# Performance work log

Hardware: AMD Instinct MI355X
Metric: run time of the kernel (lower is better)

The kernel has to match this reference:

```python
import jax, jax.numpy as jnp
import numpy as np

MAX_EDGE_LENGTH = 100.0  # filtration cap from cfg['self_supervised']['max_edge_length']


def pairwise_dist(x):
    # Euclidean pairwise distances, [N, N]
    sq = jnp.sum(x * x, axis=-1)
    d2 = sq[:, None] + sq[None, :] - 2.0 * (x @ x.T)
    return jnp.sqrt(jnp.maximum(d2, 0.0) + 1e-12)


def mst_edge_weights(D):
    """Prim's MST over dense distance matrix D [N,N]. Returns N-1 edge weights.
    These weights are exactly the H0 death times of the Vietoris-Rips filtration
    (all H0 features are born at 0)."""
    N = D.shape[0]
    dist0 = D[0]                                   # min distance from tree to each node
    in_tree0 = jnp.zeros((N,), bool).at[0].set(True)

    def step(carry, _):
        dist, in_tree = carry
        masked = jnp.where(in_tree, jnp.inf, dist)
        j = jnp.argmin(masked)
        w = masked[j]                              # weight of edge added to MST
        in_tree = in_tree.at[j].set(True)
        dist = jnp.minimum(dist, D[j])
        return (dist, in_tree), w

    _, weights = jax.lax.scan(step, (dist0, in_tree0), None, length=N - 1)
    return weights


def h0_deaths(x):
    # H0 persistence diagram deaths (births are all 0), capped at max_edge_length
    return jnp.minimum(mst_edge_weights(pairwise_dist(x)), MAX_EDGE_LENGTH)


def setup_inputs() -> dict:
    key = jax.random.key(0)
    k1, k2 = jax.random.split(key)
    N, Dm = 4096, 128
    x_1 = jax.random.normal(k1, (N, Dm), dtype=jnp.float32)
    # correlated second view, as in a siamese/self-supervised setting
    x_2 = x_1 + 0.1 * jax.random.normal(k2, (N, Dm), dtype=jnp.float32)
    return {"x_1": x_1, "x_2": x_2, "plot": 0}


def reference(x_1, x_2, plot):
    # MSE representation loss
    representation_loss = jnp.mean((x_1 - x_2) ** 2)
    # H0 persistence diagrams via Vietoris-Rips (MST formulation)
    d1 = jnp.sort(h0_deaths(x_1))
    d2 = jnp.sort(h0_deaths(x_2))
    # Wasserstein-1 distance between the two H0 diagrams (births all 0,
    # equal cardinality => optimal matching is the sorted matching of deaths)
    topological_loss = jnp.sum(jnp.abs(d1 - d2))
    return representation_loss + topological_loss
```

## Files before the change

kernel.cpp:

```cpp
#include <hip/hip_runtime.h>
#include <hip/hip_fp16.h>

#define NPT 4096
#define DM 128
#define ROUNDS 12
#define INF64 0xFFFFFFFFFFFFFFFFull
#define INF32 0xFFFFFFFFu

typedef _Float16 f16x8 __attribute__((ext_vector_type(8)));
typedef _Float16 f16x2 __attribute__((ext_vector_type(2)));
typedef float f32x4 __attribute__((ext_vector_type(4)));

static __device__ __forceinline__ unsigned long long make_key64(unsigned key, unsigned node) {
    unsigned h = key >> 16, j = key & 0xFFFFu;
    unsigned mn = node < j ? node : j;
    unsigned mx = node < j ? j : node;
    return ((unsigned long long)h << 48) | ((unsigned long long)mn << 32) |
           ((unsigned long long)mx << 16) | (unsigned long long)j;
}

__global__ __launch_bounds__(256) void init_kernel(unsigned* __restrict__ comp,
                                                   unsigned long long* __restrict__ compbest,
                                                   float* __restrict__ w,
                                                   unsigned* __restrict__ cnt,
                                                   float* __restrict__ rep) {
    int i = blockIdx.x * blockDim.x + threadIdx.x;
    comp[i] = (unsigned)(i & (NPT - 1));
    compbest[i] = INF64;
    w[i] = 0.0f;
    if (i < 2) cnt[i] = 0u;
    if (i == 0) rep[0] = 0.0f;
}

__global__ __launch_bounds__(256) void prep_kernel(const float* __restrict__ x1,
                                                   const float* __restrict__ x2,
                                                   _Float16* __restrict__ Xh,
                                                   float* __restrict__ norms,
                                                   float* __restrict__ rep) {
    const int wv = threadIdx.x >> 6, ln = threadIdx.x & 63;
    const int row = blockIdx.x * 4 + wv;
    float2 v1 = *(const float2*)(x1 + (size_t)row * DM + ln * 2);
    float2 v2 = *(const float2*)(x2 + (size_t)row * DM + ln * 2);
    _Float16 a0 = (_Float16)v1.x, a1 = (_Float16)v1.y;
    _Float16 b0 = (_Float16)v2.x, b1 = (_Float16)v2.y;
    f16x2 pa; pa[0] = a0; pa[1] = a1;
    f16x2 pb; pb[0] = b0; pb[1] = b1;
    *(f16x2*)(Xh + (size_t)row * DM + ln * 2) = pa;
    *(f16x2*)(Xh + (size_t)(NPT + row) * DM + ln * 2) = pb;

    float s1 = (float)a0 * (float)a0 + (float)a1 * (float)a1;
    float s2 = (float)b0 * (float)b0 + (float)b1 * (float)b1;
    float dx = v1.x - v2.x, dy = v1.y - v2.y;
    float rs = dx * dx + dy * dy;
    #pragma unroll
    for (int off = 32; off > 0; off >>= 1) {
        s1 += __shfl_down(s1, off);
        s2 += __shfl_down(s2, off);
        rs += __shfl_down(rs, off);
    }
    __shared__ float partial[4];
    if (ln == 0) {
        norms[row] = s1;
        norms[NPT + row] = s2;
        partial[wv] = rs;
    }
    __syncthreads();
    if (threadIdx.x == 0)
        atomicAdd(rep, partial[0] + partial[1] + partial[2] + partial[3]);
}

__global__ __launch_bounds__(256) void gram_kernel(const _Float16* __restrict__ Xh,
                                                   const float* __restrict__ norms,
                                                   __half* __restrict__ Dall,
                                                   unsigned long long* __restrict__ compbestAll) {
    const int mat = blockIdx.y;
    const _Float16* __restrict__ X = Xh + (size_t)mat * NPT * DM;
    const float* __restrict__ nrm = norms + mat * NPT;
    __half* __restrict__ D = Dall + (size_t)mat * NPT * NPT;
    unsigned long long* __restrict__ compbest = compbestAll + mat * NPT;

    const int I = blockIdx.x >> 5;
    const int J = blockIdx.x & 31;

    __shared__ __half tile[128 * 136];
    __shared__ unsigned keybuf[128 * 33];

    const int t = threadIdx.x;
    const int wv = t >> 6, ln = t & 63;
    const int rloc = (wv >> 1) * 64;
    const int cloc = (wv & 1) * 64;
    const int rowBase = I * 128 + rloc;
    const int colBase = J * 128 + cloc;
    const int lr = ln & 15;
    const int kg = ln >> 4;

    f32x4 acc[4][4];
    #pragma unroll
    for (int m = 0; m < 4; ++m)
        #pragma unroll
        for (int n = 0; n < 4; ++n)
            acc[m][n] = (f32x4){0.f, 0.f, 0.f, 0.f};

    #pragma unroll
    for (int ks = 0; ks < 4; ++ks) {
        const int k0 = ks * 32 + kg * 8;
        f16x8 a[4], b[4];
        #pragma unroll
        for (int m = 0; m < 4; ++m)
            a[m] = *(const f16x8*)(X + (size_t)(rowBase + m * 16 + lr) * DM + k0);
        #pragma unroll
        for (int n = 0; n < 4; ++n)
            b[n] = *(const f16x8*)(X + (size_t)(colBase + n * 16 + lr) * DM + k0);
        #pragma unroll
        for (int m = 0; m < 4; ++m)
            #pragma unroll
            for (int n = 0; n < 4; ++n)
                acc[m][n] = __builtin_amdgcn_mfma_f32_16x16x32_f16(a[m], b[n], acc[m][n], 0, 0, 0);
    }

    float nr[16], nc[4];
    #pragma unroll
    for (int m = 0; m < 4; ++m)
        #pragma unroll
        for (int q = 0; q < 4; ++q)
            nr[m * 4 + q] = nrm[rowBase + m * 16 + kg * 4 + q];
    #pragma unroll
    for (int n = 0; n < 4; ++n) nc[n] = nrm[colBase + n * 16 + lr];

    #pragma unroll
    for (int m = 0; m < 4; ++m) {
        #pragma unroll
        for (int q = 0; q < 4; ++q) {
            const int rl = rloc + m * 16 + kg * 4 + q;
            const int rglob = I * 128 + rl;
            unsigned best = INF32;
            #pragma unroll
            for (int n = 0; n < 4; ++n) {
                const int cl = cloc + n * 16 + lr;
                const int cglob = J * 128 + cl;
                float d2 = nr[m * 4 + q] + nc[n] - 2.0f * acc[m][n][q];
                float d = sqrtf(fmaxf(d2, 0.0f) + 1e-12f);
                __half hd = __float2half(d);
                tile[rl * 136 + cl] = hd;
                unsigned key = ((unsigned)__half_as_ushort(hd) << 16) | (unsigned)cglob;
                if (cglob == rglob) key = INF32;
                best = best < key ? best : key;
            }
            keybuf[rl * 33 + (wv & 1) * 16 + lr] = best;
        }
    }
    __syncthreads();

    {
        const int r = t >> 1, h = t & 1;
        unsigned best = INF32;
        #pragma unroll
        for (int i = 0; i < 16; ++i) {
            unsigned k = keybuf[r * 33 + h * 16 + i];
            best = best < k ? best : k;
        }
        unsigned o = __shfl_xor(best, 1);
        best = best < o ? best : o;
        if (h == 0 && best != INF32)
            atomicMin(&compbest[I * 128 + r], make_key64(best, (unsigned)(I * 128 + r)));
    }

    const int tileRow0 = I * 128;
    #pragma unroll
    for (int it = 0; it < 8; ++it) {
        int idx = it * 256 + t;
        int row = idx >> 4;
        int ch = idx & 15;
        *(uint4*)(&D[(size_t)(tileRow0 + row) * NPT + J * 128 + ch * 8]) =
            *(const uint4*)(&tile[row * 136 + ch * 8]);
    }
}

__global__ __launch_bounds__(1024) void boruvka_a2(const __half* __restrict__ Dall,
                                                   const unsigned* __restrict__ compAll,
                                                   unsigned long long* __restrict__ compbestAll,
                                                   const unsigned* __restrict__ cnt) {
    const int mat = blockIdx.y;
    if (cnt[mat] >= NPT - 1u) return;
    const __half* __restrict__ D = Dall + (size_t)mat * NPT * NPT;
    const unsigned* __restrict__ comp = compAll + mat * NPT;
    unsigned long long* __restrict__ compbest = compbestAll + mat * NPT;

    __shared__ unsigned short lcomp[NPT];
    const int t = threadIdx.x;
    for (int i = t; i < NPT; i += 1024) lcomp[i] = (unsigned short)comp[i];
    __syncthreads();

    const int wv = t >> 6, ln = t & 63;
    const int node0 = blockIdx.x * 32 + wv * 2;
    const int node1 = node0 + 1;
    const unsigned ci0 = lcomp[node0];
    const unsigned ci1 = lcomp[node1];
    const uint4* __restrict__ row0 = (const uint4*)(D + (size_t)node0 * NPT);
    const uint4* __restrict__ row1 = (const uint4*)(D + (size_t)node1 * NPT);

    uint4 d0[8], d1[8];
    #pragma unroll
    for (int k = 0; k < 8; ++k) d0[k] = row0[k * 64 + ln];
    #pragma unroll
    for (int k = 0; k < 8; ++k) d1[k] = row1[k * 64 + ln];

    unsigned best0 = INF32, best1 = INF32;
    #pragma unroll
    for (int k = 0; k < 8; ++k) {
        const int jb = (k * 64 + ln) * 8;
        uint4 cv = *(const uint4*)&lcomp[jb];
        const unsigned dp0[4] = {d0[k].x, d0[k].y, d0[k].z, d0[k].w};
        const unsigned dp1[4] = {d1[k].x, d1[k].y, d1[k].z, d1[k].w};
        const unsigned cp[4]  = {cv.x, cv.y, cv.z, cv.w};
        #pragma unroll
        for (int q = 0; q < 4; ++q) {
            int j0 = jb + q * 2;
            unsigned clo = cp[q] & 0xFFFFu, chi = cp[q] >> 16;
            unsigned k00 = (dp0[q] << 16) | (unsigned)j0;
            unsigned k01 = (dp0[q] & 0xFFFF0000u) | (unsigned)(j0 + 1);
            if (clo == ci0) k00 = INF32;
            if (chi == ci0) k01 = INF32;
            unsigned m0 = k00 < k01 ? k00 : k01;
            best0 = best0 < m0 ? best0 : m0;
            unsigned k10 = (dp1[q] << 16) | (unsigned)j0;
            unsigned k11 = (dp1[q] & 0xFFFF0000u) | (unsigned)(j0 + 1);
            if (clo == ci1) k10 = INF32;
            if (chi == ci1) k11 = INF32;
            unsigned m1 = k10 < k11 ? k10 : k11;
            best1 = best1 < m1 ? best1 : m1;
        }
    }
    #pragma unroll
    for (int off = 32; off > 0; off >>= 1) {
        unsigned o0 = __shfl_down(best0, off);
        best0 = best0 < o0 ? best0 : o0;
        unsigned o1 = __shfl_down(best1, off);
        best1 = best1 < o1 ? best1 : o1;
    }
    if (ln == 0) {
        if (best0 != INF32) atomicMin(&compbest[ci0], make_key64(best0, (unsigned)node0));
        if (best1 != INF32) atomicMin(&compbest[ci1], make_key64(best1, (unsigned)node1));
    }
}

__global__ __launch_bounds__(1024) void boruvka_cd(unsigned* __restrict__ compAll,
                                                   unsigned long long* __restrict__ compbestAll,
                                                   float* __restrict__ wAll,
                                                   unsigned* __restrict__ cntAll) {
    const int mat = blockIdx.x;
    if (cntAll[mat] >= NPT - 1u) return;
    unsigned* __restrict__ comp = compAll + mat * NPT;
    unsigned long long* __restrict__ compbest = compbestAll + mat * NPT;
    float* __restrict__ w = wAll + mat * NPT;
    unsigned* __restrict__ cnt = cntAll + mat;

    __shared__ unsigned short par[NPT];
    const int t = threadIdx.x;

    for (int c = t; c < NPT; c += 1024) {
        unsigned p = (unsigned)c;
        unsigned long long key = compbest[c];
        if (comp[c] == (unsigned)c && key != INF64) {
            unsigned jout = (unsigned)(key & 0xFFFFull);
            unsigned c2 = comp[jout];
            unsigned long long k2 = compbest[c2];
            bool mutual = (k2 >> 16) == (key >> 16);
            if (!mutual || (unsigned)c < c2) {
                unsigned short hb = (unsigned short)(key >> 48);
                float wv = fminf(__half2float(__ushort_as_half(hb)), 100.0f);
                unsigned slot = atomicAdd(cnt, 1u);
                w[slot] = wv;
            }
            p = (mutual && (unsigned)c < c2) ? (unsigned)c : c2;
        }
        par[c] = (unsigned short)p;
    }
    __syncthreads();

    for (int it = 0; it < 12; ++it) {
        unsigned short np[4];
        #pragma unroll
        for (int q = 0; q < 4; ++q) np[q] = par[par[t + q * 1024]];
        __syncthreads();
        #pragma unroll
        for (int q = 0; q < 4; ++q) par[t + q * 1024] = np[q];
        __syncthreads();
    }

    for (int c = t; c < NPT; c += 1024) {
        comp[c] = par[comp[c]];
        compbest[c] = INF64;
    }
}

__global__ __launch_bounds__(1024) void sort_kernel(float* __restrict__ wAll) {
    float* __restrict__ w = wAll + blockIdx.x * NPT;
    __shared__ float s[NPT];
    const int t = threadIdx.x;
    for (int i = t; i < NPT; i += 1024) s[i] = w[i];
    __syncthreads();

    for (int k = 2; k <= NPT; k <<= 1) {
        for (int j = k >> 1; j > 0; j >>= 1) {
            for (int i = t; i < NPT; i += 1024) {
                int ixj = i ^ j;
                if (ixj > i) {
                    bool up = (i & k) == 0;
                    float a = s[i], b = s[ixj];
                    if ((a > b) == up) { s[i] = b; s[ixj] = a; }
                }
            }
            __syncthreads();
        }
    }
    for (int i = t; i < NPT; i += 1024) w[i] = s[i];
}

__global__ __launch_bounds__(1024) void final2_kernel(const float* __restrict__ w,
                                                      const float* __restrict__ rep,
                                                      float* __restrict__ out) {
    const int t = threadIdx.x;
    float loc = 0.f;
    for (int i = t; i < NPT; i += 1024) loc += fabsf(w[i] - w[NPT + i]);
    #pragma unroll
    for (int off = 32; off > 0; off >>= 1) loc += __shfl_down(loc, off);
    __shared__ float reds[16];
    int wv = t >> 6, ln = t & 63;
    if (ln == 0) reds[wv] = loc;
    __syncthreads();
    if (t == 0) {
        float tot = 0.f;
        #pragma unroll
        for (int i = 0; i < 16; ++i) tot += reds[i];
        out[0] = tot + rep[0] * (1.0f / (NPT * DM));
    }
}

extern "C" void kernel_launch(void* const* d_in, const int* in_sizes, int n_in,
                              void* d_out, int out_size, void* d_ws, size_t ws_size,
                              hipStream_t stream) {
    const float* x1 = (const float*)d_in[0];
    const float* x2 = (const float*)d_in[1];
    float* out = (float*)d_out;

    char* ws = (char*)d_ws;
    __half* D = (__half*)ws;
    size_t off = (size_t)2 * NPT * NPT * sizeof(__half);
    _Float16* Xh = (_Float16*)(ws + off);
    off += (size_t)2 * NPT * DM * sizeof(_Float16);
    float* norms = (float*)(ws + off);
    off += (size_t)2 * NPT * sizeof(float);
    unsigned long long* compbest = (unsigned long long*)(ws + off);
    off += (size_t)2 * NPT * sizeof(unsigned long long);
    float* w = (float*)(ws + off);
    off += (size_t)2 * NPT * sizeof(float);
    unsigned* comp = (unsigned*)(ws + off);
    off += (size_t)2 * NPT * sizeof(unsigned);
    unsigned* cnt = (unsigned*)(ws + off);
    off += 2 * sizeof(unsigned);
    float* rep = (float*)(ws + off);

    init_kernel<<<2 * NPT / 256, 256, 0, stream>>>(comp, compbest, w, cnt, rep);

    prep_kernel<<<NPT / 4, 256, 0, stream>>>(x1, x2, Xh, norms, rep);

    gram_kernel<<<dim3(1024, 2), 256, 0, stream>>>(Xh, norms, D, compbest);

    boruvka_cd<<<2, 1024, 0, stream>>>(comp, compbest, w, cnt);

    for (int r = 1; r < ROUNDS; ++r) {
        boruvka_a2<<<dim3(NPT / 32, 2), 1024, 0, stream>>>(D, comp, compbest, cnt);
        boruvka_cd<<<2, 1024, 0, stream>>>(comp, compbest, w, cnt);
    }

    sort_kernel<<<2, 1024, 0, stream>>>(w);

    final2_kernel<<<1, 1024, 0, stream>>>(w, rep, out);
}
```

Before: 347.8 us.

## Track per-node second-best neighbor to skip full Boruvka row scans on alternate rounds

The gram kernel now records, for each row, the two smallest distance keys per column tile. A new reduction kernel turns these into best and second-best candidates per node. Boruvka rounds then alternate between a full row scan that keeps the top two keys in distinct components and a cheap pairA pass. That pass reuses the stored candidates and only rescans the row when both fall inside the node's own component. The aim is to cut the number of full passes over the 2x32MB fp16 distance matrix. In exchange the full scans carry extra per-lane state and shuffle work, and more kernels are launched.

```diff
diff --git a/kernel.cpp b/kernel.cpp
--- a/kernel.cpp
+++ b/kernel.cpp
@@ -3,7 +3,6 @@
 
 #define NPT 4096
 #define DM 128
-#define ROUNDS 12
 #define INF64 0xFFFFFFFFFFFFFFFFull
 #define INF32 0xFFFFFFFFu
 
@@ -18,6 +17,15 @@
     return ((unsigned long long)h << 48) | ((unsigned long long)mn << 32) |
            ((unsigned long long)mx << 16) | (unsigned long long)j;
 }
+
+#define UPD(K1, C1, K2, C2, kk, cc)                                   \
+    do {                                                              \
+        unsigned _k = (kk), _c = (cc);                                \
+        if (_k < K1) {                                                \
+            if (_c != C1) { K2 = K1; C2 = C1; }                       \
+            K1 = _k; C1 = _c;                                         \
+        } else if (_k < K2 && _c != C1) { K2 = _k; C2 = _c; }         \
+    } while (0)
 
 __global__ __launch_bounds__(256) void init_kernel(unsigned* __restrict__ comp,
                                                    unsigned long long* __restrict__ compbest,
@@ -72,18 +80,18 @@
 __global__ __launch_bounds__(256) void gram_kernel(const _Float16* __restrict__ Xh,
                                                    const float* __restrict__ norms,
                                                    __half* __restrict__ Dall,
-                                                   unsigned long long* __restrict__ compbestAll) {
+                                                   unsigned* __restrict__ Gall) {
     const int mat = blockIdx.y;
     const _Float16* __restrict__ X = Xh + (size_t)mat * NPT * DM;
     const float* __restrict__ nrm = norms + mat * NPT;
     __half* __restrict__ D = Dall + (size_t)mat * NPT * NPT;
-    unsigned long long* __restrict__ compbest = compbestAll + mat * NPT;
+    unsigned* __restrict__ G = Gall + (size_t)mat * NPT * 64;
 
     const int I = blockIdx.x >> 5;
     const int J = blockIdx.x & 31;
 
     __shared__ __half tile[128 * 136];
-    __shared__ unsigned keybuf[128 * 33];
+    __shared__ unsigned keybuf[128 * 66];
 
     const int t = threadIdx.x;
     const int wv = t >> 6, ln = t & 63;
@@ -133,7 +141,7 @@
         for (int q = 0; q < 4; ++q) {
             const int rl = rloc + m * 16 + kg * 4 + q;
             const int rglob = I * 128 + rl;
-            unsigned best = INF32;
+            unsigned b = INF32, s = INF32;
             #pragma unroll
             for (int n = 0; n < 4; ++n) {
                 const int cl = cloc + n * 16 + lr;
@@ -144,26 +152,38 @@
                 tile[rl * 136 + cl] = hd;
                 unsigned key = ((unsigned)__half_as_ushort(hd) << 16) | (unsigned)cglob;
                 if (cglob == rglob) key = INF32;
-                best = best < key ? best : key;
+                if (key < b) { s = b; b = key; } else if (key < s) s = key;
             }
-            keybuf[rl * 33 + (wv & 1) * 16 + lr] = best;
+            keybuf[rl * 66 + (wv & 1) * 16 + lr] = b;
+            keybuf[rl * 66 + 33 + (wv & 1) * 16 + lr] = s;
         }
     }
     __syncthreads();
 
     {
         const int r = t >> 1, h = t & 1;
-        unsigned best = INF32;
+        unsigned B = INF32, S = INF32;
         #pragma unroll
         for (int i = 0; i < 16; ++i) {
-            unsigned k = keybuf[r * 33 + h * 16 + i];
-            best = best < k ? best : k;
-        }
-        unsigned o = __shfl_xor(best, 1);
-        best = best < o ? best : o;
-        if (h == 0 && best != INF32)
-            atomicMin(&compbest[I * 128 + r], make_key64(best, (unsigned)(I * 128 + r)));
-    }
+            unsigned k = keybuf[r * 66 + h * 16 + i];
+            if (k < B) { S = B; B = k; } else if (k < S) S = k;
+        }
+        #pragma unroll
+        for (int i = 0; i < 16; ++i) {
+            unsigned k = keybuf[r * 66 + 33 + h * 16 + i];
+            if (k < B) { S = B; B = k; } else if (k < S) S = k;
+        }
+        unsigned oB = __shfl_xor(B, 1), oS = __shfl_xor(S, 1);
+        unsigned wn = B < oB ? B : oB;
+        unsigned ls = B < oB ? oB : B;
+        unsigned ws = B < oB ? S : oS;
+        B = wn; S = ls < ws ? ls : ws;
+        if (h == 0) {
+            G[(size_t)(I * 128 + r) * 64 + J * 2] = B;
+            G[(size_t)(I * 128 + r) * 64 + J * 2 + 1] = S;
+        }
+    }
+    __syncthreads();
 
     const int tileRow0 = I * 128;
     #pragma unroll
@@ -176,15 +196,47 @@
     }
 }
 
-__global__ __launch_bounds__(1024) void boruvka_a2(const __half* __restrict__ Dall,
-                                                   const unsigned* __restrict__ compAll,
-                                                   unsigned long long* __restrict__ compbestAll,
-                                                   const unsigned* __restrict__ cnt) {
+__global__ __launch_bounds__(1024) void greduce_kernel(const unsigned* __restrict__ Gall,
+                                                       unsigned long long* __restrict__ compbestAll,
+                                                       unsigned long long* __restrict__ bndAll) {
+    const int mat = blockIdx.y;
+    const unsigned* __restrict__ G = Gall + (size_t)mat * NPT * 64;
+    unsigned long long* __restrict__ compbest = compbestAll + mat * NPT;
+    unsigned long long* __restrict__ bnd = bndAll + mat * NPT;
+    const int t = threadIdx.x, wv = t >> 6, ln = t & 63;
+    #pragma unroll
+    for (int rr = 0; rr < 4; ++rr) {
+        const int row = blockIdx.x * 64 + wv * 4 + rr;
+        unsigned B = G[(size_t)row * 64 + ln];
+        unsigned S = INF32;
+        #pragma unroll
+        for (int off = 32; off > 0; off >>= 1) {
+            unsigned oB = __shfl_down(B, off), oS = __shfl_down(S, off);
+            unsigned wn = B < oB ? B : oB;
+            unsigned ls = B < oB ? oB : B;
+            unsigned ws = B < oB ? S : oS;
+            B = wn;
+            unsigned m2 = ls < ws ? ls : ws;
+            S = m2;
+        }
+        if (ln == 0) {
+            compbest[row] = make_key64(B, (unsigned)row);
+            bnd[row] = ((unsigned long long)B << 32) | S;
+        }
+    }
+}
+
+__global__ __launch_bounds__(1024) void scan_s2(const __half* __restrict__ Dall,
+                                                const unsigned* __restrict__ compAll,
+                                                unsigned long long* __restrict__ compbestAll,
+                                                unsigned long long* __restrict__ bndAll,
+                                                const unsigned* __restrict__ cnt) {
     const int mat = blockIdx.y;
     if (cnt[mat] >= NPT - 1u) return;
     const __half* __restrict__ D = Dall + (size_t)mat * NPT * NPT;
     const unsigned* __restrict__ comp = compAll + mat * NPT;
     unsigned long long* __restrict__ compbest = compbestAll + mat * NPT;
+    unsigned long long* __restrict__ bnd = bndAll + mat * NPT;
 
     __shared__ unsigned short lcomp[NPT];
     const int t = threadIdx.x;
@@ -199,19 +251,17 @@
     const uint4* __restrict__ row0 = (const uint4*)(D + (size_t)node0 * NPT);
     const uint4* __restrict__ row1 = (const uint4*)(D + (size_t)node1 * NPT);
 
-    uint4 d0[8], d1[8];
-    #pragma unroll
-    for (int k = 0; k < 8; ++k) d0[k] = row0[k * 64 + ln];
-    #pragma unroll
-    for (int k = 0; k < 8; ++k) d1[k] = row1[k * 64 + ln];
-
-    unsigned best0 = INF32, best1 = INF32;
+    unsigned K1a = INF32, C1a = 0xFFFFu, K2a = INF32, C2a = 0xFFFFu;
+    unsigned K1b = INF32, C1b = 0xFFFFu, K2b = INF32, C2b = 0xFFFFu;
+
     #pragma unroll
     for (int k = 0; k < 8; ++k) {
+        uint4 d0 = row0[k * 64 + ln];
+        uint4 d1 = row1[k * 64 + ln];
         const int jb = (k * 64 + ln) * 8;
         uint4 cv = *(const uint4*)&lcomp[jb];
-        const unsigned dp0[4] = {d0[k].x, d0[k].y, d0[k].z, d0[k].w};
-        const unsigned dp1[4] = {d1[k].x, d1[k].y, d1[k].z, d1[k].w};
+        const unsigned dp0[4] = {d0.x, d0.y, d0.z, d0.w};
+        const unsigned dp1[4] = {d1.x, d1.y, d1.z, d1.w};
         const unsigned cp[4]  = {cv.x, cv.y, cv.z, cv.w};
         #pragma unroll
         for (int q = 0; q < 4; ++q) {
@@ -221,26 +271,116 @@
             unsigned k01 = (dp0[q] & 0xFFFF0000u) | (unsigned)(j0 + 1);
             if (clo == ci0) k00 = INF32;
             if (chi == ci0) k01 = INF32;
-            unsigned m0 = k00 < k01 ? k00 : k01;
-            best0 = best0 < m0 ? best0 : m0;
+            UPD(K1a, C1a, K2a, C2a, k00, clo);
+            UPD(K1a, C1a, K2a, C2a, k01, chi);
             unsigned k10 = (dp1[q] << 16) | (unsigned)j0;
             unsigned k11 = (dp1[q] & 0xFFFF0000u) | (unsigned)(j0 + 1);
             if (clo == ci1) k10 = INF32;
             if (chi == ci1) k11 = INF32;
-            unsigned m1 = k10 < k11 ? k10 : k11;
-            best1 = best1 < m1 ? best1 : m1;
-        }
-    }
+            UPD(K1b, C1b, K2b, C2b, k10, clo);
+            UPD(K1b, C1b, K2b, C2b, k11, chi);
+        }
+    }
+
     #pragma unroll
     for (int off = 32; off > 0; off >>= 1) {
-        unsigned o0 = __shfl_down(best0, off);
-        best0 = best0 < o0 ? best0 : o0;
-        unsigned o1 = __shfl_down(best1, off);
-        best1 = best1 < o1 ? best1 : o1;
-    }
+        unsigned oK1, oC1, oK2, oC2, X, XC;
+        oK1 = __shfl_down(K1a, off); oC1 = __shfl_down(C1a, off);
+        oK2 = __shfl_down(K2a, off); oC2 = __shfl_down(C2a, off);
+        if (oK1 < K1a) {
+            X = (C1a != oC1) ? K1a : K2a; XC = (C1a != oC1) ? C1a : C2a;
+            if (oK2 <= X) { K2a = oK2; C2a = oC2; } else { K2a = X; C2a = XC; }
+            K1a = oK1; C1a = oC1;
+        } else {
+            X = (oC1 != C1a) ? oK1 : oK2; XC = (oC1 != C1a) ? oC1 : oC2;
+            if (X < K2a) { K2a = X; C2a = XC; }
+        }
+        oK1 = __shfl_down(K1b, off); oC1 = __shfl_down(C1b, off);
+        oK2 = __shfl_down(K2b, off); oC2 = __shfl_down(C2b, off);
+        if (oK1 < K1b) {
+            X = (C1b != oC1) ? K1b : K2b; XC = (C1b != oC1) ? C1b : C2b;
+            if (oK2 <= X) { K2b = oK2; C2b = oC2; } else { K2b = X; C2b = XC; }
+            K1b = oK1; C1b = oC1;
+        } else {
+            X = (oC1 != C1b) ? oK1 : oK2; XC = (oC1 != C1b) ? oC1 : oC2;
+            if (X < K2b) { K2b = X; C2b = XC; }
+        }
+    }
+
     if (ln == 0) {
-        if (best0 != INF32) atomicMin(&compbest[ci0], make_key64(best0, (unsigned)node0));
-        if (best1 != INF32) atomicMin(&compbest[ci1], make_key64(best1, (unsigned)node1));
+        if (K1a != INF32) atomicMin(&compbest[ci0], make_key64(K1a, (unsigned)node0));
+        if (K1b != INF32) atomicMin(&compbest[ci1], make_key64(K1b, (unsigned)node1));
+        bnd[node0] = ((unsigned long long)K1a << 32) | K2a;
+        bnd[node1] = ((unsigned long long)K1b << 32) | K2b;
+    }
+}
+
+__global__ __launch_bounds__(1024) void pairA(const __half* __restrict__ Dall,
+                                              const unsigned* __restrict__ compAll,
+                                              unsigned long long* __restrict__ compbestAll,
+                                              const unsigned long long* __restrict__ bndAll,
+                                              const unsigned* __restrict__ cnt) {
+    const int mat = blockIdx.y;
+    if (cnt[mat] >= NPT - 1u) return;
+    const __half* __restrict__ D = Dall + (size_t)mat * NPT * NPT;
+    const unsigned* __restrict__ comp = compAll + mat * NPT;
+    unsigned long long* __restrict__ compbest = compbestAll + mat * NPT;
+    const unsigned long long* __restrict__ bnd = bndAll + mat * NPT;
+
+    __shared__ unsigned short lcomp[NPT];
+    const int t = threadIdx.x;
+    for (int i = t; i < NPT; i += 1024) lcomp[i] = (unsigned short)comp[i];
+    __syncthreads();
+
+    const int wv = t >> 6, ln = t & 63;
+    #pragma unroll
+    for (int rr = 0; rr < 4; ++rr) {
+        const int node = blockIdx.x * 64 + wv * 4 + rr;
+        const unsigned ci = lcomp[node];
+        unsigned long long bv = bnd[node];
+        unsigned K1 = (unsigned)(bv >> 32), K2 = (unsigned)bv;
+        unsigned cand = INF32;
+        bool fb = false;
+        if (K1 != INF32) {
+            unsigned c1 = lcomp[K1 & 0xFFFFu];
+            if (c1 != ci) cand = K1;
+            else if (K2 != INF32) {
+                unsigned c2 = lcomp[K2 & 0xFFFFu];
+                if (c2 != ci) cand = K2;
+                else fb = true;
+            }
+        }
+        if (cand != INF32) {
+            if (ln == 0) atomicMin(&compbest[ci], make_key64(cand, (unsigned)node));
+        } else if (fb) {
+            const uint4* __restrict__ row = (const uint4*)(D + (size_t)node * NPT);
+            unsigned best = INF32;
+            #pragma unroll
+            for (int k = 0; k < 8; ++k) {
+                uint4 dv = row[k * 64 + ln];
+                const int jb = (k * 64 + ln) * 8;
+                uint4 cv = *(const uint4*)&lcomp[jb];
+                const unsigned dp[4] = {dv.x, dv.y, dv.z, dv.w};
+                const unsigned cp[4] = {cv.x, cv.y, cv.z, cv.w};
+                #pragma unroll
+                for (int q = 0; q < 4; ++q) {
+                    int j0 = jb + q * 2;
+                    unsigned k0 = (dp[q] << 16) | (unsigned)j0;
+                    unsigned k1 = (dp[q] & 0xFFFF0000u) | (unsigned)(j0 + 1);
+                    if ((cp[q] & 0xFFFFu) == ci) k0 = INF32;
+                    if ((cp[q] >> 16) == ci)     k1 = INF32;
+                    unsigned m = k0 < k1 ? k0 : k1;
+                    best = best < m ? best : m;
+                }
+            }
+            #pragma unroll
+            for (int off = 32; off > 0; off >>= 1) {
+                unsigned o = __shfl_down(best, off);
+                best = best < o ? best : o;
+            }
+            if (ln == 0 && best != INF32)
+                atomicMin(&compbest[ci], make_key64(best, (unsigned)node));
+        }
     }
 }
 
@@ -353,10 +493,14 @@
     off += (size_t)2 * NPT * sizeof(float);
     unsigned long long* compbest = (unsigned long long*)(ws + off);
     off += (size_t)2 * NPT * sizeof(unsigned long long);
+    unsigned long long* bnd = (unsigned long long*)(ws + off);
+    off += (size_t)2 * NPT * sizeof(unsigned long long);
     float* w = (float*)(ws + off);
     off += (size_t)2 * NPT * sizeof(float);
     unsigned* comp = (unsigned*)(ws + off);
     off += (size_t)2 * NPT * sizeof(unsigned);
+    unsigned* G = (unsigned*)(ws + off);
+    off += (size_t)2 * NPT * 64 * sizeof(unsigned);
     unsigned* cnt = (unsigned*)(ws + off);
     off += 2 * sizeof(unsigned);
     float* rep = (float*)(ws + off);
@@ -365,13 +509,19 @@
 
     prep_kernel<<<NPT / 4, 256, 0, stream>>>(x1, x2, Xh, norms, rep);
 
-    gram_kernel<<<dim3(1024, 2), 256, 0, stream>>>(Xh, norms, D, compbest);
-
+    gram_kernel<<<dim3(1024, 2), 256, 0, stream>>>(Xh, norms, D, G);
+
+    greduce_kernel<<<dim3(NPT / 64, 2), 1024, 0, stream>>>(G, compbest, bnd);
     boruvka_cd<<<2, 1024, 0, stream>>>(comp, compbest, w, cnt);
 
-    for (int r = 1; r < ROUNDS; ++r) {
-        boruvka_a2<<<dim3(NPT / 32, 2), 1024, 0, stream>>>(D, comp, compbest, cnt);
+    pairA<<<dim3(NPT / 64, 2), 1024, 0, stream>>>(D, comp, compbest, bnd, cnt);
+    boruvka_cd<<<2, 1024, 0, stream>>>(comp, compbest, w, cnt);
+
+    for (int s = 0; s < 5; ++s) {
+        scan_s2<<<dim3(NPT / 32, 2), 1024, 0, stream>>>(D, comp, compbest, bnd, cnt);
         boruvka_cd<<<2, 1024, 0, stream>>>(comp, compbest, w, cnt);
+        pairA<<<dim3(NPT / 64, 2), 1024, 0, stream>>>(D, comp, compbest, bnd, cnt);
+        boruvka_cd<<<2, 1024, 0, stream>>>(comp, compbest, w, cnt);
     }
 
     sort_kernel<<<2, 1024, 0, stream>>>(w);
```

New measurement: 342.1 us. No clear change (-1.6%).
